# Performance work log

Measured on AMD Instinct MI355X. Metric: run time of the kernel, lower is better.

## Reference

```python
import jax, jax.numpy as jnp
import numpy as np

B, T, D = 4, 2048, 1024
H, HS = 16, 64  # num heads, head size; H*HS == D


def setup_inputs() -> dict:
    key = jax.random.key(0)
    ks = jax.random.split(key, 6)
    scale = D ** -0.5
    x = jax.random.normal(ks[0], (B, T, D), dtype=jnp.float32)
    # per-head projections, stacked: [H, D, HS]
    Wq = jax.random.normal(ks[1], (H, D, HS), dtype=jnp.float32) * scale
    Wk = jax.random.normal(ks[2], (H, D, HS), dtype=jnp.float32) * scale
    Wv = jax.random.normal(ks[3], (H, D, HS), dtype=jnp.float32) * scale
    # output projection: [H*HS, D] + bias [D]
    Wp = jax.random.normal(ks[4], (H * HS, D), dtype=jnp.float32) * ((H * HS) ** -0.5)
    bp = jax.random.normal(ks[5], (D,), dtype=jnp.float32) * 0.01
    return {"x": x, "Wq": Wq, "Wk": Wk, "Wv": Wv, "Wp": Wp, "bp": bp}


def reference(x, Wq, Wk, Wv, Wp, bp):
    # per-head Q, K, V projections (batched over heads): [B, H, T, HS]
    q = jnp.einsum('btd,hde->bhte', x, Wq)
    k = jnp.einsum('btd,hde->bhte', x, Wk)
    v = jnp.einsum('btd,hde->bhte', x, Wv)
    # scaled scores with causal mask: [B, H, T, T]
    scores = jnp.einsum('bhte,bhse->bhts', q, k) * (HS ** -0.5)
    causal = jnp.tril(jnp.ones((T, T), dtype=bool))
    scores = jnp.where(causal, scores, jnp.float32(-jnp.inf))
    wei = jax.nn.softmax(scores, axis=-1)  # dropout is identity at eval
    out = jnp.einsum('bhts,bhse->bhte', wei, v)
    # concat heads -> [B, T, H*HS], then output projection
    out = out.transpose(0, 2, 1, 3).reshape(B, T, H * HS)
    return out @ Wp + bp
```

## Files before the change

kernel.cpp:

```cpp
#include <hip/hip_runtime.h>
#include <stdint.h>

typedef __attribute__((ext_vector_type(8))) short short8;
typedef __attribute__((ext_vector_type(4))) float f32x4;
typedef __attribute__((ext_vector_type(16))) float f32x16;

__device__ __forceinline__ unsigned short f2bf(float f) {
  unsigned u = __float_as_uint(f);
  u = u + 0x7FFFu + ((u >> 16) & 1u);
  return (unsigned short)(u >> 16);
}
__device__ __forceinline__ unsigned cvtpk_bf16(float lo, float hi) {
  unsigned r;
  asm("v_cvt_pk_bf16_f32 %0, %1, %2" : "=v"(r) : "v"(lo), "v"(hi));
  return r;
}
__device__ __forceinline__ void gl2lds16(const void* g, void* l) {
  __builtin_amdgcn_global_load_lds(
      (const __attribute__((address_space(1))) void*)(uintptr_t)g,
      (__attribute__((address_space(3))) void*)(uintptr_t)l, 16, 0, 0);
}

__global__ __launch_bounds__(256) void pack_x_kernel(const float* __restrict__ x,
                                                     ushort* __restrict__ xb) {
  int i = (blockIdx.x * 256 + threadIdx.x) * 8;
  float4 a = *(const float4*)(x + i);
  float4 b = *(const float4*)(x + i + 4);
  uint4 o;
  o.x = (unsigned)f2bf(a.x) | ((unsigned)f2bf(a.y) << 16);
  o.y = (unsigned)f2bf(a.z) | ((unsigned)f2bf(a.w) << 16);
  o.z = (unsigned)f2bf(b.x) | ((unsigned)f2bf(b.y) << 16);
  o.w = (unsigned)f2bf(b.z) | ((unsigned)f2bf(b.w) << 16);
  *(uint4*)(xb + i) = o;
}

__global__ __launch_bounds__(256) void pack_w_kernel(const float* __restrict__ Wq,
                                                     const float* __restrict__ Wk,
                                                     const float* __restrict__ Wv,
                                                     const float* __restrict__ Wp,
                                                     ushort* __restrict__ WqkvT,
                                                     ushort* __restrict__ WpT) {
  __shared__ float tile[64][65];
  const int bid = blockIdx.x;
  const int tid = threadIdx.x;
  const int lr = tid >> 6;
  const int lc = tid & 63;
  if (bid < 768) {
    const int s = bid >> 8;
    const int rem = bid & 255;
    const int h = rem >> 4;
    const int dt = rem & 15;
    const float* W = (s == 0) ? Wq : (s == 1) ? Wk : Wv;
#pragma unroll
    for (int p = 0; p < 16; ++p) {
      int r = p * 4 + lr;
      tile[r][lc] = W[(size_t)(h * 1024 + dt * 64 + r) * 64 + lc];
    }
    __syncthreads();
#pragma unroll
    for (int p = 0; p < 16; ++p) {
      int e = p * 4 + lr;
      float v = tile[lc][e];
      WqkvT[(size_t)(s * 1024 + h * 64 + e) * 1024 + dt * 64 + lc] = f2bf(v);
    }
  } else {
    const int t = bid - 768;
    const int rt = t >> 4, ct = t & 15;
#pragma unroll
    for (int p = 0; p < 16; ++p) {
      int r = p * 4 + lr;
      tile[r][lc] = Wp[(size_t)(rt * 64 + r) * 1024 + ct * 64 + lc];
    }
    __syncthreads();
#pragma unroll
    for (int p = 0; p < 16; ++p) {
      int c = p * 4 + lr;
      float v = tile[lc][c];
      WpT[(size_t)(ct * 64 + c) * 1024 + rt * 64 + lc] = f2bf(v);
    }
  }
}

template <int OUT_MODE>
__global__ __launch_bounds__(256) void gemm_bt(const ushort* __restrict__ A,
                                               const ushort* __restrict__ BT,
                                               ushort* __restrict__ Cb,
                                               float* __restrict__ Cf,
                                               const float* __restrict__ bias,
                                               int M, int N, int K) {
  __shared__ __align__(16) ushort Al[128 * 32];
  __shared__ __align__(16) ushort Bl[128 * 32];
  const int tid = threadIdx.x;
  const int lane = tid & 63;
  const int wave = tid >> 6;
  const int wm = wave >> 1, wn = wave & 1;
  const int nbx = gridDim.x;
  const int nwg = nbx * gridDim.y;
  int wg = blockIdx.y * nbx + blockIdx.x;
  wg = (wg & 7) * (nwg >> 3) + (wg >> 3);
  const int m0 = (wg / nbx) * 128, n0 = (wg % nbx) * 128;
  const int r16 = lane & 15, g = lane >> 4;
  f32x4 acc[4][4] = {};
  const int kTiles = K >> 5;
  const size_t ldb = (size_t)K * 2;
  const int srow = tid >> 2;
  const int srb = (tid & 3) * 16;
  const char* a_src = (const char*)A + (size_t)(m0 + srow) * ldb + srb;
  const char* b_src = (const char*)BT + (size_t)(n0 + srow) * ldb + srb;
  char* a_dst = (char*)Al + wave * 1024;
  char* b_dst = (char*)Bl + wave * 1024;
  for (int kt = 0; kt < kTiles; ++kt) {
    const int k0b = kt * 64;
    if (kt) __syncthreads();
    gl2lds16(a_src + k0b, a_dst);
    gl2lds16(a_src + (size_t)64 * ldb + k0b, a_dst + 4096);
    gl2lds16(b_src + k0b, b_dst);
    gl2lds16(b_src + (size_t)64 * ldb + k0b, b_dst + 4096);
    __syncthreads();
    short8 af[4], bfr[4];
#pragma unroll
    for (int i = 0; i < 4; ++i) {
      af[i] = *(const short8*)(Al + ((wm * 64 + i * 16 + r16) * 32 + g * 8));
      bfr[i] = *(const short8*)(Bl + ((wn * 64 + i * 16 + r16) * 32 + g * 8));
    }
#pragma unroll
    for (int mi = 0; mi < 4; ++mi)
#pragma unroll
      for (int ni = 0; ni < 4; ++ni)
        acc[mi][ni] =
            __builtin_amdgcn_mfma_f32_16x16x32_bf16(af[mi], bfr[ni], acc[mi][ni], 0, 0, 0);
  }
#pragma unroll
  for (int mi = 0; mi < 4; ++mi)
#pragma unroll
    for (int ni = 0; ni < 4; ++ni)
#pragma unroll
      for (int r = 0; r < 4; ++r) {
        int row = m0 + wm * 64 + mi * 16 + g * 4 + r;
        int col = n0 + wn * 64 + ni * 16 + r16;
        float v = acc[mi][ni][r];
        if (OUT_MODE == 0) {
          Cb[(size_t)row * N + col] = f2bf(v);
        } else {
          Cf[(size_t)row * N + col] = v + bias[col];
        }
      }
}

__global__ __launch_bounds__(256) void attn_mfma_kernel(const ushort* __restrict__ QKV,
                                                        ushort* __restrict__ O) {
  int flat = blockIdx.z * 128 + blockIdx.y * 8 + blockIdx.x;
  flat = (flat & 7) * 64 + (flat >> 3);
  const int qtA = flat & 7;
  const int h = (flat >> 3) & 15;
  const int b = flat >> 7;
  __shared__ __align__(16) ushort Kl[64 * 64];
  __shared__ __align__(16) ushort VT[64 * 64];
  const int tid = threadIdx.x;
  const int lane = tid & 63;
  const int wave = tid >> 6;
  const int lo5 = lane & 31;
  const int hi = lane >> 5;

#pragma unroll
  for (int ph = 0; ph < 2; ++ph) {
    const int qt = ph ? qtA : (15 - qtA);
    const int qbase = qt * 128 + wave * 32;

    short8 qf[4];
    {
      const ushort* qp = QKV + ((size_t)(b * 2048 + qbase + lo5) * 3072) + h * 64 + hi * 8;
#pragma unroll
      for (int dc = 0; dc < 4; ++dc) qf[dc] = *(const short8*)(qp + dc * 16);
    }

    f32x16 o0 = {}, o1 = {};
    float l_acc = 0.f;

    const int nblk = qt * 2 + 2;
    for (int blk = 0; blk < nblk; ++blk) {
      const int s0 = blk * 64;
      __syncthreads();
      {
        const int key = tid & 63, ch = tid >> 6;
        const ushort* kp =
            QKV + ((size_t)(b * 2048 + s0 + key) * 3072) + 1024 + h * 64 + ch * 16;
        uint4 k0 = *(const uint4*)kp;
        uint4 k1 = *(const uint4*)(kp + 8);
        char* dst = (char*)Kl + key * 128;
        const int sw = (key & 7) << 4;
        *(uint4*)(dst + ((ch * 32) ^ sw)) = k0;
        *(uint4*)(dst + ((ch * 32 + 16) ^ sw)) = k1;
      }
      {
        const int kp2 = (tid & 31) * 2;
        const int dg = tid >> 5;
        const ushort* vp =
            QKV + ((size_t)(b * 2048 + s0 + kp2) * 3072) + 2048 + h * 64 + dg * 8;
        uint4 v0 = *(const uint4*)vp;
        uint4 v1 = *(const uint4*)(vp + 3072);
        const ushort* e0 = (const ushort*)&v0;
        const ushort* e1 = (const ushort*)&v1;
#pragma unroll
        for (int j = 0; j < 8; ++j) {
          const int row = dg * 8 + j;
          *(unsigned*)((char*)VT + row * 128 + ((kp2 * 2) ^ ((row & 7) << 4))) =
              (unsigned)e0[j] | ((unsigned)e1[j] << 16);
        }
      }
      __syncthreads();

#pragma unroll
      for (int g2 = 0; g2 < 2; ++g2) {
        f32x16 s_acc = {};
        const int krow = g2 * 32 + lo5;
        const char* ksrc = (const char*)Kl + krow * 128;
        const int ksw = (krow & 7) << 4;
#pragma unroll
        for (int dc = 0; dc < 4; ++dc) {
          short8 kf = *(const short8*)(ksrc + ((dc * 32 + hi * 16) ^ ksw));
          s_acc = __builtin_amdgcn_mfma_f32_32x32x16_bf16(kf, qf[dc], s_acc, 0, 0, 0);
        }
        float p[16];
        const int qg = qbase + lo5;
        const int ksg = s0 + g2 * 32 + 4 * hi;
#pragma unroll
        for (int r = 0; r < 16; ++r) {
          const int key_g = ksg + (r & 3) + 8 * (r >> 2);
          float pv = __expf(s_acc[r] * 0.125f);
          pv = (key_g <= qg) ? pv : 0.f;
          p[r] = pv;
          l_acc += pv;
        }
#pragma unroll
        for (int kc = 0; kc < 2; ++kc) {
          unsigned w0 = cvtpk_bf16(p[kc * 8 + 0], p[kc * 8 + 1]);
          unsigned w2 = cvtpk_bf16(p[kc * 8 + 4], p[kc * 8 + 5]);
          unsigned w1 = cvtpk_bf16(p[kc * 8 + 2], p[kc * 8 + 3]);
          unsigned w3 = cvtpk_bf16(p[kc * 8 + 6], p[kc * 8 + 7]);
          asm("v_permlane32_swap_b32 %0, %1" : "+v"(w0), "+v"(w2));
          asm("v_permlane32_swap_b32 %0, %1" : "+v"(w1), "+v"(w3));
          uint4 paw;
          paw.x = w0; paw.y = w1; paw.z = w2; paw.w = w3;
          short8 pa = *(short8*)&paw;
          const int kb = (g2 * 32 + kc * 16 + hi * 8) * 2;
          {
            const int vrow = lo5;
            short8 vf =
                *(const short8*)((const char*)VT + vrow * 128 + (kb ^ ((vrow & 7) << 4)));
            o0 = __builtin_amdgcn_mfma_f32_32x32x16_bf16(pa, vf, o0, 0, 0, 0);
          }
          {
            const int vrow = 32 + lo5;
            short8 vf =
                *(const short8*)((const char*)VT + vrow * 128 + (kb ^ ((vrow & 7) << 4)));
            o1 = __builtin_amdgcn_mfma_f32_32x32x16_bf16(pa, vf, o1, 0, 0, 0);
          }
        }
      }
    }
    l_acc += __shfl_xor(l_acc, 32);
    const float linv = 1.f / l_acc;
#pragma unroll
    for (int r = 0; r < 16; ++r) {
      const int qr = (r & 3) + 8 * (r >> 2) + 4 * hi;
      const float li = __shfl(linv, qr);
      ushort* ob = O + ((size_t)(b * 2048 + qbase + qr) * 1024) + h * 64 + lo5;
      ob[0] = f2bf(o0[r] * li);
      ob[32] = f2bf(o1[r] * li);
    }
  }
}

extern "C" void kernel_launch(void* const* d_in, const int* in_sizes, int n_in,
                              void* d_out, int out_size, void* d_ws, size_t ws_size,
                              hipStream_t stream) {
  const float* x = (const float*)d_in[0];
  const float* Wq = (const float*)d_in[1];
  const float* Wk = (const float*)d_in[2];
  const float* Wv = (const float*)d_in[3];
  const float* Wp = (const float*)d_in[4];
  const float* bp = (const float*)d_in[5];
  float* out = (float*)d_out;

  ushort* xb = (ushort*)d_ws;
  ushort* WqkvT = xb + 8388608;
  ushort* WpT = WqkvT + 3145728;
  ushort* QKV = WpT + 1048576;
  ushort* O = QKV + 25165824;

  pack_x_kernel<<<4096, 256, 0, stream>>>(x, xb);
  pack_w_kernel<<<1024, 256, 0, stream>>>(Wq, Wk, Wv, Wp, WqkvT, WpT);
  gemm_bt<0><<<dim3(24, 64), 256, 0, stream>>>(xb, WqkvT, QKV, nullptr, nullptr,
                                               8192, 3072, 1024);
  attn_mfma_kernel<<<dim3(8, 16, 4), 256, 0, stream>>>(QKV, O);
  gemm_bt<1><<<dim3(8, 64), 256, 0, stream>>>(O, WpT, nullptr, out, bp,
                                              8192, 1024, 1024);
}
```

Before: 188.3 us.

## Prefetch V registers, async-load K to LDS, fold softmax scale into Wq, skip masked tiles

The softmax scale and log2(e) factor are folded into the bf16-packed Wq, so the attention kernel can use a raw exp2 instead of scaling and calling __expf. K tiles are now loaded straight into swizzled LDS with global_load_lds, and the next V block is prefetched into registers while the current block computes. Key sub-tiles that lie wholly above the causal diagonal are skipped, and the per-element mask is applied only to diagonal sub-tiles. Folding the scale into the bf16 weights changes rounding slightly, and the extra prefetch registers may reduce occupancy.

```diff
diff --git a/kernel.cpp b/kernel.cpp
--- a/kernel.cpp
+++ b/kernel.cpp
@@ -14,6 +14,13 @@
   unsigned r;
   asm("v_cvt_pk_bf16_f32 %0, %1, %2" : "=v"(r) : "v"(lo), "v"(hi));
   return r;
+}
+__device__ __forceinline__ float fast_exp2(float x) {
+#if __has_builtin(__builtin_amdgcn_exp2f)
+  return __builtin_amdgcn_exp2f(x);
+#else
+  return exp2f(x);
+#endif
 }
 __device__ __forceinline__ void gl2lds16(const void* g, void* l) {
   __builtin_amdgcn_global_load_lds(
@@ -51,6 +58,7 @@
     const int h = rem >> 4;
     const int dt = rem & 15;
     const float* W = (s == 0) ? Wq : (s == 1) ? Wk : Wv;
+    const float scale = (s == 0) ? 0.18033688011f : 1.0f;
 #pragma unroll
     for (int p = 0; p < 16; ++p) {
       int r = p * 4 + lr;
@@ -60,7 +68,7 @@
 #pragma unroll
     for (int p = 0; p < 16; ++p) {
       int e = p * 4 + lr;
-      float v = tile[lc][e];
+      float v = tile[lc][e] * scale;
       WqkvT[(size_t)(s * 1024 + h * 64 + e) * 1024 + dt * 64 + lc] = f2bf(v);
     }
   } else {
@@ -162,10 +170,20 @@
   const int lo5 = lane & 31;
   const int hi = lane >> 5;
 
+  const int k_key0 = wave * 16 + (lane >> 3);
+  const int k_key1 = k_key0 + 8;
+  const int ksrc_off0 = ((lane & 7) * 16) ^ ((k_key0 & 7) << 4);
+  const int ksrc_off1 = ((lane & 7) * 16) ^ ((k_key1 & 7) << 4);
+  const char* kgbase = (const char*)(QKV + ((size_t)b * 2048) * 3072 + 1024 + h * 64);
+  const int kp2 = (tid & 31) * 2;
+  const int dg = tid >> 5;
+  const char* vgbase = (const char*)(QKV + ((size_t)b * 2048) * 3072 + 2048 + h * 64 + dg * 8);
+
 #pragma unroll
   for (int ph = 0; ph < 2; ++ph) {
     const int qt = ph ? qtA : (15 - qtA);
     const int qbase = qt * 128 + wave * 32;
+    const int qg = qbase + lo5;
 
     short8 qf[4];
     {
@@ -176,31 +194,21 @@
 
     f32x16 o0 = {}, o1 = {};
     float l_acc = 0.f;
-
     const int nblk = qt * 2 + 2;
+
+    uint4 nv0, nv1;
+    {
+      const char* vp = vgbase + (size_t)kp2 * 6144;
+      nv0 = *(const uint4*)(vp);
+      nv1 = *(const uint4*)(vp + 6144);
+    }
+
     for (int blk = 0; blk < nblk; ++blk) {
       const int s0 = blk * 64;
       __syncthreads();
       {
-        const int key = tid & 63, ch = tid >> 6;
-        const ushort* kp =
-            QKV + ((size_t)(b * 2048 + s0 + key) * 3072) + 1024 + h * 64 + ch * 16;
-        uint4 k0 = *(const uint4*)kp;
-        uint4 k1 = *(const uint4*)(kp + 8);
-        char* dst = (char*)Kl + key * 128;
-        const int sw = (key & 7) << 4;
-        *(uint4*)(dst + ((ch * 32) ^ sw)) = k0;
-        *(uint4*)(dst + ((ch * 32 + 16) ^ sw)) = k1;
-      }
-      {
-        const int kp2 = (tid & 31) * 2;
-        const int dg = tid >> 5;
-        const ushort* vp =
-            QKV + ((size_t)(b * 2048 + s0 + kp2) * 3072) + 2048 + h * 64 + dg * 8;
-        uint4 v0 = *(const uint4*)vp;
-        uint4 v1 = *(const uint4*)(vp + 3072);
-        const ushort* e0 = (const ushort*)&v0;
-        const ushort* e1 = (const ushort*)&v1;
+        const ushort* e0 = (const ushort*)&nv0;
+        const ushort* e1 = (const ushort*)&nv1;
 #pragma unroll
         for (int j = 0; j < 8; ++j) {
           const int row = dg * 8 + j;
@@ -208,10 +216,21 @@
               (unsigned)e0[j] | ((unsigned)e1[j] << 16);
         }
       }
+      gl2lds16(kgbase + (size_t)(s0 + k_key0) * 6144 + ksrc_off0, (char*)Kl + wave * 2048);
+      gl2lds16(kgbase + (size_t)(s0 + k_key1) * 6144 + ksrc_off1,
+               (char*)Kl + wave * 2048 + 1024);
       __syncthreads();
 
+      if (blk + 1 < nblk) {
+        const char* vp = vgbase + (size_t)(s0 + 64 + kp2) * 6144;
+        nv0 = *(const uint4*)(vp);
+        nv1 = *(const uint4*)(vp + 6144);
+      }
+
 #pragma unroll
       for (int g2 = 0; g2 < 2; ++g2) {
+        const int ks = s0 + g2 * 32;
+        if (ks > qbase + 31) continue;
         f32x16 s_acc = {};
         const int krow = g2 * 32 + lo5;
         const char* ksrc = (const char*)Kl + krow * 128;
@@ -222,15 +241,23 @@
           s_acc = __builtin_amdgcn_mfma_f32_32x32x16_bf16(kf, qf[dc], s_acc, 0, 0, 0);
         }
         float p[16];
-        const int qg = qbase + lo5;
-        const int ksg = s0 + g2 * 32 + 4 * hi;
-#pragma unroll
-        for (int r = 0; r < 16; ++r) {
-          const int key_g = ksg + (r & 3) + 8 * (r >> 2);
-          float pv = __expf(s_acc[r] * 0.125f);
-          pv = (key_g <= qg) ? pv : 0.f;
-          p[r] = pv;
-          l_acc += pv;
+        if (ks + 31 > qbase) {
+          const int ksg = ks + 4 * hi;
+#pragma unroll
+          for (int r = 0; r < 16; ++r) {
+            const int key_g = ksg + (r & 3) + 8 * (r >> 2);
+            float pv = fast_exp2(s_acc[r]);
+            pv = (key_g <= qg) ? pv : 0.f;
+            p[r] = pv;
+            l_acc += pv;
+          }
+        } else {
+#pragma unroll
+          for (int r = 0; r < 16; ++r) {
+            float pv = fast_exp2(s_acc[r]);
+            p[r] = pv;
+            l_acc += pv;
+          }
         }
 #pragma unroll
         for (int kc = 0; kc < 2; ++kc) {
@@ -259,6 +286,7 @@
         }
       }
     }
+
     l_acc += __shfl_xor(l_acc, 32);
     const float linv = 1.f / l_acc;
 #pragma unroll
```

New measurement: 171.6 us. 8.9% less time.
